# Kernel tuning notes

Hardware: AMD Instinct MI355X
Metric: run time of the kernel (lower is better)

The kernel has to match this reference:

```python
import jax, jax.numpy as jnp
import numpy as np

B, S, D = 16, 4096, 128
FACTOR = 1


def setup_inputs() -> dict:
    key = jax.random.key(0)
    kq, kk, kv = jax.random.split(key, 3)
    Q = jax.random.normal(kq, (B, S, D), dtype=jnp.float32)
    K = jax.random.normal(kk, (B, S, D), dtype=jnp.float32)
    V = jax.random.normal(kv, (B, S, D), dtype=jnp.float32)
    return {"Q": Q, "K": K, "V": V}


def reference(Q, K, V):
    # [B, S, D] -> [B, D, S] (head dim of 1 is elided; all ops are per-(b,d) lane)
    Qc = jnp.transpose(Q, (0, 2, 1))
    Kc = jnp.transpose(K, (0, 2, 1))
    Vc = jnp.transpose(V, (0, 2, 1))
    seq_len = Qc.shape[-1]
    # FFT cross-correlation: corr[b,d,tau] = sum_t Q[b,d,t] K[b,d,t-tau] (circular)
    corr = jnp.fft.irfft(
        jnp.fft.rfft(Qc, axis=-1) * jnp.conj(jnp.fft.rfft(Kc, axis=-1)),
        n=seq_len, axis=-1)  # [B, D, S]
    top_k = int(FACTOR * np.log(seq_len))  # = 8 for S=4096
    weights, delay = jax.lax.top_k(corr, top_k)  # [B, D, K], raw corr values (no softmax)
    # time-delay aggregation: roll V circularly by each selected delay and weighted-sum
    t = jnp.arange(seq_len)
    idx = (delay[..., None] + t[None, None, None, :]) % seq_len  # [B, D, K, S]
    pattern = jnp.take_along_axis(Vc[:, :, None, :], idx, axis=-1)  # [B, D, K, S]
    out = jnp.einsum('bdks,bdk->bds', pattern, weights)  # [B, D, S]
    # dropout is identity at inference
    return jnp.transpose(out, (0, 2, 1))  # [B, S, D]
```

## Files before the change

### kernel.cpp

```cpp
#include <hip/hip_runtime.h>
#include <math.h>

#define SEQ 4096
#define LOG2SEQ 12
#define TOPK 8
#define NB 16
#define ND 128
#define NEGINF (-3.402823466e+38f)

#define PADF(i) ((i) + ((i) >> 5))

#define TPITCH 68

__device__ __forceinline__ int rev12(int x) {
    return (int)(__brev((unsigned)x) >> (32 - LOG2SEQ));
}

__device__ __forceinline__ void twid(int idx, float& c, float& s) {
    const float a = (float)idx * (-0.001533980787885641f);
    c = __cosf(a);
    s = __sinf(a);
}

__device__ __forceinline__ void transpose64_body(const float* __restrict__ inb,
                                                 float* __restrict__ outb,
                                                 int R, int C) {
    __shared__ float lds[64 * TPITCH];
    const int tid = threadIdx.x;
    const int c0 = blockIdx.x * 64, r0 = blockIdx.y * 64;
    const int q = tid & 15;
    const int rr = tid >> 4;
#pragma unroll
    for (int pass = 0; pass < 4; ++pass) {
        const int r = pass * 16 + rr;
        const float4 v =
            *(const float4*)(inb + (size_t)(r0 + r) * C + (c0 + 4 * q));
        const int base = (4 * q) * TPITCH + r;
        lds[base] = v.x;
        lds[base + TPITCH] = v.y;
        lds[base + 2 * TPITCH] = v.z;
        lds[base + 3 * TPITCH] = v.w;
    }
    __syncthreads();
#pragma unroll
    for (int pass = 0; pass < 4; ++pass) {
        const int c = pass * 16 + rr;
        const float4 v = *(const float4*)(lds + c * TPITCH + 4 * q);
        *(float4*)(outb + (size_t)(c0 + c) * R + (r0 + 4 * q)) = v;
    }
}

__global__ __launch_bounds__(256) void transpose3_k(const float* __restrict__ Q,
                                                    const float* __restrict__ K,
                                                    const float* __restrict__ V,
                                                    float* __restrict__ Qt,
                                                    float* __restrict__ Kt,
                                                    float* __restrict__ Vt) {
    const int which = blockIdx.z / NB;
    const int b = blockIdx.z % NB;
    const size_t bo = (size_t)b * SEQ * ND;
    const float* in = (which == 0) ? Q : (which == 1) ? K : V;
    float* out = (which == 0) ? Qt : (which == 1) ? Kt : Vt;
    transpose64_body(in + bo, out + bo, SEQ, ND);
}

__global__ __launch_bounds__(256) void transpose_back_k(const float* __restrict__ in,
                                                        float* __restrict__ out) {
    const size_t bo = (size_t)blockIdx.z * SEQ * ND;
    transpose64_body(in + bo, out + bo, ND, SEQ);
}

__global__ __launch_bounds__(256) void corr_topk_agg_k(const float* Qt,
                                                       const float* __restrict__ Kt,
                                                       const float* __restrict__ Vt,
                                                       float* Ot) {
    __shared__ float re[SEQ + SEQ / 32];
    __shared__ float im[SEQ + SEQ / 32];
    __shared__ float sval[4];
    __shared__ int sidx[4];
    __shared__ float wsel[TOPK];
    __shared__ int dsel[TOPK];

    const int tid = threadIdx.x;
    const size_t row = (size_t)blockIdx.x * SEQ;

    {
        const float4* Q4 = (const float4*)(Qt + row);
        const float4* K4 = (const float4*)(Kt + row);
        for (int t = tid; t < SEQ / 4; t += 256) {
            const float4 q = Q4[t];
            const float4 k = K4[t];
            const int b0 = PADF(4 * t);
            re[b0] = q.x; re[b0 + 1] = q.y; re[b0 + 2] = q.z; re[b0 + 3] = q.w;
            im[b0] = k.x; im[b0 + 1] = k.y; im[b0 + 2] = k.z; im[b0 + 3] = k.w;
        }
    }
    __syncthreads();

    for (int h = 2048; h >= 2; h >>= 2) {
        const int hh = h >> 1;
        const int sA = SEQ / (2 * h);
        for (int g = tid; g < SEQ / 4; g += 256) {
            const int pos = g & (hh - 1);
            const int i0 = ((g - pos) << 2) + pos;
            const int p0 = PADF(i0), p1 = PADF(i0 + hh);
            const int p2 = PADF(i0 + h), p3 = PADF(i0 + h + hh);
            const float e0r = re[p0], e0i = im[p0];
            const float e1r = re[p1], e1i = im[p1];
            const float e2r = re[p2], e2i = im[p2];
            const float e3r = re[p3], e3i = im[p3];
            float c1, s1;
            twid(pos * sA, c1, s1);
            const float cB = c1 * c1 - s1 * s1;
            const float sB = 2.0f * s1 * c1;
            const float f0r = e0r + e2r, f0i = e0i + e2i;
            float dr = e0r - e2r, di = e0i - e2i;
            const float f2r = dr * c1 - di * s1, f2i = dr * s1 + di * c1;
            const float f1r = e1r + e3r, f1i = e1i + e3i;
            dr = e1r - e3r;
            di = e1i - e3i;
            const float f3r = dr * s1 + di * c1;
            const float f3i = di * s1 - dr * c1;
            re[p0] = f0r + f1r;
            im[p0] = f0i + f1i;
            dr = f0r - f1r;
            di = f0i - f1i;
            re[p1] = dr * cB - di * sB;
            im[p1] = dr * sB + di * cB;
            re[p2] = f2r + f3r;
            im[p2] = f2i + f3i;
            dr = f2r - f3r;
            di = f2i - f3i;
            re[p3] = dr * cB - di * sB;
            im[p3] = dr * sB + di * cB;
        }
        __syncthreads();
    }

    float ar_[9], ai_[9], br_[9], bi_[9];
#pragma unroll
    for (int q = 0; q < 9; ++q) {
        const int f = tid + (q << 8);
        if (f <= SEQ / 2) {
            const int pa = PADF(rev12(f));
            const int pb = PADF(rev12((SEQ - f) & (SEQ - 1)));
            ar_[q] = re[pa];
            ai_[q] = im[pa];
            br_[q] = re[pb];
            bi_[q] = im[pb];
        }
    }
    __syncthreads();
#pragma unroll
    for (int q = 0; q < 9; ++q) {
        const int f = tid + (q << 8);
        if (f <= SEQ / 2) {
            const float ar = ar_[q], ai = ai_[q], br = br_[q], bi = bi_[q];
            const float Qr = 0.5f * (ar + br), Qi = 0.5f * (ai - bi);
            const float Kr = 0.5f * (ai + bi), Ki = 0.5f * (br - ar);
            const float invS = 1.0f / (float)SEQ;
            const float Pr = (Qr * Kr + Qi * Ki) * invS;
            const float Pi = (Qi * Kr - Qr * Ki) * invS;
            const int pa = PADF(rev12(f));
            const int pb = PADF(rev12((SEQ - f) & (SEQ - 1)));
            re[pa] = Pr;
            im[pa] = Pi;
            re[pb] = Pr;
            im[pb] = -Pi;
        }
    }
    __syncthreads();

    for (int hh = 1; hh <= 1024; hh <<= 2) {
        const int sB = SEQ / (4 * hh);
        for (int g = tid; g < SEQ / 4; g += 256) {
            const int pos = g & (hh - 1);
            const int i0 = ((g - pos) << 2) + pos;
            const int p0 = PADF(i0), p1 = PADF(i0 + hh);
            const int p2 = PADF(i0 + 2 * hh), p3 = PADF(i0 + 3 * hh);
            const float e0r = re[p0], e0i = im[p0];
            const float e1r = re[p1], e1i = im[p1];
            const float e2r = re[p2], e2i = im[p2];
            const float e3r = re[p3], e3i = im[p3];
            float cB0, sB0;
            twid(pos * sB, cB0, sB0);
            const float cA = cB0 * cB0 - sB0 * sB0;
            const float sAv = -2.0f * sB0 * cB0;
            const float cB = cB0;
            const float sBv = -sB0;
            float tr = e1r * cA - e1i * sAv, ti = e1r * sAv + e1i * cA;
            const float f0r = e0r + tr, f0i = e0i + ti;
            const float f1r = e0r - tr, f1i = e0i - ti;
            tr = e3r * cA - e3i * sAv;
            ti = e3r * sAv + e3i * cA;
            const float f2r = e2r + tr, f2i = e2i + ti;
            const float f3r = e2r - tr, f3i = e2i - ti;
            tr = f2r * cB - f2i * sBv;
            ti = f2r * sBv + f2i * cB;
            re[p0] = f0r + tr;
            im[p0] = f0i + ti;
            re[p2] = f0r - tr;
            im[p2] = f0i - ti;
            tr = -f3r * sBv - f3i * cB;
            ti = f3r * cB - f3i * sBv;
            re[p1] = f1r + tr;
            im[p1] = f1i + ti;
            re[p3] = f1r - tr;
            im[p3] = f1i - ti;
        }
        __syncthreads();
    }

    {
        const float4* V4 = (const float4*)(Vt + row);
        for (int t = tid; t < SEQ / 4; t += 256) {
            const float4 v = V4[t];
            const int b0 = PADF(4 * t);
            im[b0] = v.x; im[b0 + 1] = v.y; im[b0 + 2] = v.z; im[b0 + 3] = v.w;
        }
    }

    float vals[16];
#pragma unroll
    for (int j = 0; j < 16; ++j) {
        vals[j] = re[PADF(tid + (j << 8))];
    }
    for (int it = 0; it < TOPK; ++it) {
        float best = NEGINF;
        int bidx = 0;
#pragma unroll
        for (int j = 0; j < 16; ++j) {
            const int t = tid + (j << 8);
            if (vals[j] > best) {
                best = vals[j];
                bidx = t;
            }
        }
#pragma unroll
        for (int off = 32; off > 0; off >>= 1) {
            const float ov = __shfl_down(best, off);
            const int oi = __shfl_down(bidx, off);
            if (ov > best || (ov == best && oi < bidx)) {
                best = ov;
                bidx = oi;
            }
        }
        if ((tid & 63) == 0) {
            sval[tid >> 6] = best;
            sidx[tid >> 6] = bidx;
        }
        __syncthreads();
        if (tid == 0) {
            float bv = sval[0];
            int bi2 = sidx[0];
#pragma unroll
            for (int w = 1; w < 4; ++w) {
                const float ov = sval[w];
                const int oi = sidx[w];
                if (ov > bv || (ov == bv && oi < bi2)) {
                    bv = ov;
                    bi2 = oi;
                }
            }
            wsel[it] = bv;
            dsel[it] = bi2;
        }
        __syncthreads();
        const int win = dsel[it];
#pragma unroll
        for (int j = 0; j < 16; ++j) {
            if (tid + (j << 8) == win) vals[j] = NEGINF;
        }
    }

    float w[TOPK];
    int dl[TOPK];
#pragma unroll
    for (int k = 0; k < TOPK; ++k) {
        w[k] = wsel[k];
        dl[k] = dsel[k];
    }
    for (int j = 0; j < SEQ / 256; ++j) {
        const int t = tid + (j << 8);
        float acc = 0.0f;
#pragma unroll
        for (int k = 0; k < TOPK; ++k) {
            acc += w[k] * im[PADF((t + dl[k]) & (SEQ - 1))];
        }
        Ot[row + t] = acc;
    }
}

extern "C" void kernel_launch(void* const* d_in, const int* in_sizes, int n_in,
                              void* d_out, int out_size, void* d_ws, size_t ws_size,
                              hipStream_t stream) {
    const float* Q = (const float*)d_in[0];
    const float* K = (const float*)d_in[1];
    const float* V = (const float*)d_in[2];
    float* out = (float*)d_out;

    const size_t n = (size_t)NB * ND * SEQ;
    float* Qt = (float*)d_ws;
    float* Kt = Qt + n;
    float* Vt = Kt + n;

    dim3 g1(ND / 64, SEQ / 64, 3 * NB);
    hipLaunchKernelGGL(transpose3_k, g1, dim3(256), 0, stream, Q, K, V, Qt, Kt, Vt);

    hipLaunchKernelGGL(corr_topk_agg_k, dim3(NB * ND), dim3(256), 0, stream,
                       Qt, Kt, Vt, Qt);

    dim3 g3(SEQ / 64, ND / 64, NB);
    hipLaunchKernelGGL(transpose_back_k, g3, dim3(256), 0, stream, Qt, out);
}
```

Before: 242.3 us.

## Switch shared-memory FFT passes from radix-4 to radix-8 butterflies

Replaces the radix-4 DIF forward and DIT inverse FFT stages with radix-8 butterflies. For 4096 points this cuts the pass count from 6 to 4, which means fewer LDS read/write sweeps and fewer block-wide barriers. Each pass still needs only one sincos per butterfly; the other twiddles come from squaring and the constant 1/sqrt2 rotation. The cost is more registers per thread, and the extra twiddle squaring may slightly change rounding.

New measurement: 232.0 us. 4.3% less time.

```diff
diff --git a/kernel.cpp b/kernel.cpp
--- a/kernel.cpp
+++ b/kernel.cpp
@@ -7,6 +7,7 @@
 #define NB 16
 #define ND 128
 #define NEGINF (-3.402823466e+38f)
+#define RSQ2 0.70710678118654752f
 
 #define PADF(i) ((i) + ((i) >> 5))
 
@@ -21,6 +22,11 @@
     c = __cosf(a);
     s = __sinf(a);
 }
+
+#define CMUL(tr, ti, xr, xi, wr, wi) \
+    { tr = (xr) * (wr) - (xi) * (wi); ti = (xr) * (wi) + (xi) * (wr); }
+#define CMULC(tr, ti, xr, xi, wr, wi) \
+    { tr = (xr) * (wr) + (xi) * (wi); ti = (xi) * (wr) - (xr) * (wi); }
 
 __device__ __forceinline__ void transpose64_body(const float* __restrict__ inb,
                                                  float* __restrict__ outb,
@@ -97,42 +103,59 @@
     }
     __syncthreads();
 
-    for (int h = 2048; h >= 2; h >>= 2) {
-        const int hh = h >> 1;
-        const int sA = SEQ / (2 * h);
-        for (int g = tid; g < SEQ / 4; g += 256) {
-            const int pos = g & (hh - 1);
-            const int i0 = ((g - pos) << 2) + pos;
-            const int p0 = PADF(i0), p1 = PADF(i0 + hh);
-            const int p2 = PADF(i0 + h), p3 = PADF(i0 + h + hh);
-            const float e0r = re[p0], e0i = im[p0];
-            const float e1r = re[p1], e1i = im[p1];
-            const float e2r = re[p2], e2i = im[p2];
-            const float e3r = re[p3], e3i = im[p3];
+    for (int h = 2048; h >= 4; h >>= 3) {
+        const int hq = h >> 2;
+        const int sA = SEQ / (8 * hq);
+        for (int g = tid; g < SEQ / 8; g += 256) {
+            const int pos = g & (hq - 1);
+            const int i0 = ((g - pos) << 3) + pos;
+            int p[8];
+#pragma unroll
+            for (int j = 0; j < 8; ++j) p[j] = PADF(i0 + j * hq);
+            float er[8], ei[8];
+#pragma unroll
+            for (int j = 0; j < 8; ++j) { er[j] = re[p[j]]; ei[j] = im[p[j]]; }
             float c1, s1;
             twid(pos * sA, c1, s1);
-            const float cB = c1 * c1 - s1 * s1;
-            const float sB = 2.0f * s1 * c1;
-            const float f0r = e0r + e2r, f0i = e0i + e2i;
-            float dr = e0r - e2r, di = e0i - e2i;
-            const float f2r = dr * c1 - di * s1, f2i = dr * s1 + di * c1;
-            const float f1r = e1r + e3r, f1i = e1i + e3i;
-            dr = e1r - e3r;
-            di = e1i - e3i;
-            const float f3r = dr * s1 + di * c1;
-            const float f3i = di * s1 - dr * c1;
-            re[p0] = f0r + f1r;
-            im[p0] = f0i + f1i;
-            dr = f0r - f1r;
-            di = f0i - f1i;
-            re[p1] = dr * cB - di * sB;
-            im[p1] = dr * sB + di * cB;
-            re[p2] = f2r + f3r;
-            im[p2] = f2i + f3i;
-            dr = f2r - f3r;
-            di = f2i - f3i;
-            re[p3] = dr * cB - di * sB;
-            im[p3] = dr * sB + di * cB;
+            const float c2 = c1 * c1 - s1 * s1, s2 = 2.0f * s1 * c1;
+            const float c4 = c2 * c2 - s2 * s2, s4 = 2.0f * s2 * c2;
+            const float t1r = RSQ2 * (c1 + s1), t1i = RSQ2 * (s1 - c1);
+            float ar[8], ai[8];
+#pragma unroll
+            for (int j = 0; j < 4; ++j) {
+                ar[j] = er[j] + er[j + 4];
+                ai[j] = ei[j] + ei[j + 4];
+            }
+            float dr, di;
+            dr = er[0] - er[4]; di = ei[0] - ei[4];
+            CMUL(ar[4], ai[4], dr, di, c1, s1);
+            dr = er[1] - er[5]; di = ei[1] - ei[5];
+            CMUL(ar[5], ai[5], dr, di, t1r, t1i);
+            dr = er[2] - er[6]; di = ei[2] - ei[6];
+            CMUL(ar[6], ai[6], dr, di, s1, -c1);
+            dr = er[3] - er[7]; di = ei[3] - ei[7];
+            CMUL(ar[7], ai[7], dr, di, t1i, -t1r);
+            float br[8], bi[8];
+#pragma unroll
+            for (int base = 0; base < 8; base += 4) {
+                br[base] = ar[base] + ar[base + 2];
+                bi[base] = ai[base] + ai[base + 2];
+                dr = ar[base] - ar[base + 2]; di = ai[base] - ai[base + 2];
+                CMUL(br[base + 2], bi[base + 2], dr, di, c2, s2);
+                br[base + 1] = ar[base + 1] + ar[base + 3];
+                bi[base + 1] = ai[base + 1] + ai[base + 3];
+                dr = ar[base + 1] - ar[base + 3]; di = ai[base + 1] - ai[base + 3];
+                CMUL(br[base + 3], bi[base + 3], dr, di, s2, -c2);
+            }
+#pragma unroll
+            for (int j = 0; j < 8; j += 2) {
+                const float sr = br[j] + br[j + 1], si = bi[j] + bi[j + 1];
+                dr = br[j] - br[j + 1]; di = bi[j] - bi[j + 1];
+                float or_, oi_;
+                CMUL(or_, oi_, dr, di, c4, s4);
+                re[p[j]] = sr; im[p[j]] = si;
+                re[p[j + 1]] = or_; im[p[j + 1]] = oi_;
+            }
         }
         __syncthreads();
     }
@@ -171,42 +194,52 @@
     }
     __syncthreads();
 
-    for (int hh = 1; hh <= 1024; hh <<= 2) {
-        const int sB = SEQ / (4 * hh);
-        for (int g = tid; g < SEQ / 4; g += 256) {
-            const int pos = g & (hh - 1);
-            const int i0 = ((g - pos) << 2) + pos;
-            const int p0 = PADF(i0), p1 = PADF(i0 + hh);
-            const int p2 = PADF(i0 + 2 * hh), p3 = PADF(i0 + 3 * hh);
-            const float e0r = re[p0], e0i = im[p0];
-            const float e1r = re[p1], e1i = im[p1];
-            const float e2r = re[p2], e2i = im[p2];
-            const float e3r = re[p3], e3i = im[p3];
-            float cB0, sB0;
-            twid(pos * sB, cB0, sB0);
-            const float cA = cB0 * cB0 - sB0 * sB0;
-            const float sAv = -2.0f * sB0 * cB0;
-            const float cB = cB0;
-            const float sBv = -sB0;
-            float tr = e1r * cA - e1i * sAv, ti = e1r * sAv + e1i * cA;
-            const float f0r = e0r + tr, f0i = e0i + ti;
-            const float f1r = e0r - tr, f1i = e0i - ti;
-            tr = e3r * cA - e3i * sAv;
-            ti = e3r * sAv + e3i * cA;
-            const float f2r = e2r + tr, f2i = e2i + ti;
-            const float f3r = e2r - tr, f3i = e2i - ti;
-            tr = f2r * cB - f2i * sBv;
-            ti = f2r * sBv + f2i * cB;
-            re[p0] = f0r + tr;
-            im[p0] = f0i + ti;
-            re[p2] = f0r - tr;
-            im[p2] = f0i - ti;
-            tr = -f3r * sBv - f3i * cB;
-            ti = f3r * cB - f3i * sBv;
-            re[p1] = f1r + tr;
-            im[p1] = f1i + ti;
-            re[p3] = f1r - tr;
-            im[p3] = f1i - ti;
+    for (int hq = 1; hq <= 512; hq <<= 3) {
+        const int sA = SEQ / (8 * hq);
+        for (int g = tid; g < SEQ / 8; g += 256) {
+            const int pos = g & (hq - 1);
+            const int i0 = ((g - pos) << 3) + pos;
+            int p[8];
+#pragma unroll
+            for (int j = 0; j < 8; ++j) p[j] = PADF(i0 + j * hq);
+            float er[8], ei[8];
+#pragma unroll
+            for (int j = 0; j < 8; ++j) { er[j] = re[p[j]]; ei[j] = im[p[j]]; }
+            float c1, s1;
+            twid(pos * sA, c1, s1);
+            const float c2 = c1 * c1 - s1 * s1, s2 = 2.0f * s1 * c1;
+            const float c4 = c2 * c2 - s2 * s2, s4 = 2.0f * s2 * c2;
+            const float u1r = RSQ2 * (c1 + s1), u1i = RSQ2 * (c1 - s1);
+            float tr, ti;
+            float ar[8], ai[8];
+#pragma unroll
+            for (int j = 0; j < 8; j += 2) {
+                CMULC(tr, ti, er[j + 1], ei[j + 1], c4, s4);
+                ar[j] = er[j] + tr; ai[j] = ei[j] + ti;
+                ar[j + 1] = er[j] - tr; ai[j + 1] = ei[j] - ti;
+            }
+            float br[8], bi[8];
+#pragma unroll
+            for (int base = 0; base < 8; base += 4) {
+                CMULC(tr, ti, ar[base + 2], ai[base + 2], c2, s2);
+                br[base] = ar[base] + tr; bi[base] = ai[base] + ti;
+                br[base + 2] = ar[base] - tr; bi[base + 2] = ai[base] - ti;
+                CMUL(tr, ti, ar[base + 3], ai[base + 3], s2, c2);
+                br[base + 1] = ar[base + 1] + tr; bi[base + 1] = ai[base + 1] + ti;
+                br[base + 3] = ar[base + 1] - tr; bi[base + 3] = ai[base + 1] - ti;
+            }
+            CMULC(tr, ti, br[4], bi[4], c1, s1);
+            re[p[0]] = br[0] + tr; im[p[0]] = bi[0] + ti;
+            re[p[4]] = br[0] - tr; im[p[4]] = bi[0] - ti;
+            CMUL(tr, ti, br[5], bi[5], u1r, u1i);
+            re[p[1]] = br[1] + tr; im[p[1]] = bi[1] + ti;
+            re[p[5]] = br[1] - tr; im[p[5]] = bi[1] - ti;
+            CMUL(tr, ti, br[6], bi[6], s1, c1);
+            re[p[2]] = br[2] + tr; im[p[2]] = bi[2] + ti;
+            re[p[6]] = br[2] - tr; im[p[6]] = bi[2] - ti;
+            CMUL(tr, ti, br[7], bi[7], -u1i, u1r);
+            re[p[3]] = br[3] + tr; im[p[3]] = bi[3] + ti;
+            re[p[7]] = br[3] - tr; im[p[7]] = bi[3] - ti;
         }
         __syncthreads();
     }
```
